# Kernel tuning notes

Measured on AMD Instinct MI355X. Metric: run time of the kernel, lower is better.

The kernel has to match this reference:

```python
import jax, jax.numpy as jnp
import numpy as np

B, N1, N2 = 4, 16384, 4096   # scenes, fine points/scene, coarse points/scene
CIN, COUT = 512, 256
K = 3
EPS_BN = 1e-5
EPS_D = 1e-8


def setup_inputs() -> dict:
    key = jax.random.key(0)
    ks = jax.random.split(key, 6)
    return {
        "point_1": jax.random.uniform(ks[0], (B * N1, 3), dtype=jnp.float32),
        "feat_1": jax.random.normal(ks[1], (B * N1, COUT), dtype=jnp.float32) * 0.1,
        "point_2": jax.random.uniform(ks[2], (B * N2, 3), dtype=jnp.float32),
        "feat_2": jax.random.normal(ks[3], (B * N2, CIN), dtype=jnp.float32) * 0.1,
        "W1": jax.random.normal(ks[4], (COUT, COUT), dtype=jnp.float32) / np.sqrt(COUT).astype(np.float32),
        "b1": jnp.zeros((COUT,), jnp.float32),
        "g1": jnp.ones((COUT,), jnp.float32),
        "beta1": jnp.zeros((COUT,), jnp.float32),
        "W2": jax.random.normal(ks[5], (CIN, COUT), dtype=jnp.float32) / np.sqrt(CIN).astype(np.float32),
        "b2": jnp.zeros((COUT,), jnp.float32),
        "g2": jnp.ones((COUT,), jnp.float32),
        "beta2": jnp.zeros((COUT,), jnp.float32),
        # equal-sized segments: row_splits = [0, N, 2N, ...]
        "row_splits_1": jnp.arange(B + 1, dtype=jnp.int32) * N1,
        "row_splits_2": jnp.arange(B + 1, dtype=jnp.int32) * N2,
    }


def _bn(x, gamma, beta):
    # BatchNorm1d, training mode (biased variance, as in torch)
    mu = x.mean(0)
    var = x.var(0)
    return gamma * (x - mu) * jax.lax.rsqrt(var + EPS_BN) + beta


def reference(point_1, feat_1, point_2, feat_2,
              W1, b1, g1, beta1, W2, b2, g2, beta2,
              row_splits_1, row_splits_2):
    # linear1(feat_1): Linear + BN + ReLU
    f1 = jax.nn.relu(_bn(feat_1 @ W1 + b1, g1, beta1))          # [B*N1, COUT]
    # linear2(feat_2): Linear + BN + ReLU
    f2 = jax.nn.relu(_bn(feat_2 @ W2 + b2, g2, beta2))          # [B*N2, COUT]

    # batched KNN (equal row_splits -> reshape into [B, n, 3])
    q = point_1.reshape(B, N1, 3)
    p = point_2.reshape(B, N2, 3)
    d2 = ((q * q).sum(-1)[:, :, None]
          + (p * p).sum(-1)[:, None, :]
          - 2.0 * jnp.einsum("bnd,bmd->bnm", q, p))             # [B, N1, N2] squared dists
    neg_d, idx = jax.lax.top_k(-d2, K)                           # [B, N1, K]
    dist = jnp.maximum(-neg_d, 0.0)

    # inverse-distance weights (knn search is non-differentiable in the original)
    recip = 1.0 / (dist + EPS_D)
    w = jax.lax.stop_gradient(recip / recip.sum(-1, keepdims=True))  # [B, N1, K]

    # gather + weighted sum (three-interpolate)
    f2b = f2.reshape(B, N2, COUT)
    gathered = f2b[jnp.arange(B)[:, None, None], idx]            # [B, N1, K, COUT]
    interp = (gathered * w[..., None]).sum(2).reshape(B * N1, COUT)

    return f1 + interp
```

## Files before the change

### kernel.cpp

```cpp
#include <hip/hip_runtime.h>
#include <hip/hip_bf16.h>
#include <math.h>

#define N1R 65536
#define N2R 16384
#define NPB 4096
#define NQB 16384
#define CC  256
#define ASTRIDE 40
#define NCELL 512
#define GRID_FAIL_R2 0.015625f

typedef __attribute__((ext_vector_type(4))) float v4f;
typedef __attribute__((ext_vector_type(8))) short v8s;

static __device__ __forceinline__ short f2bs(float f) {
    union { __hip_bfloat16 h; short s; } u;
    u.h = __float2bfloat16(f);
    return u.s;
}

static __device__ __forceinline__ int cell_of(float x, float y, float z) {
    const int cx = min(7, (int)(x * 8.0f));
    const int cy = min(7, (int)(y * 8.0f));
    const int cz = min(7, (int)(z * 8.0f));
    return (cz << 6) | (cy << 3) | cx;
}

static __device__ __forceinline__ void ins3(float d, int si,
    float& b0, float& b1, float& b2, int& i0, int& i1, int& i2)
{
    const bool lt0 = (d < b0) | ((d == b0) & (si < i0));
    const bool lt1 = (d < b1) | ((d == b1) & (si < i1));
    const bool lt2 = (d < b2) | ((d == b2) & (si < i2));
    b2 = lt1 ? b1 : (lt2 ? d : b2);   i2 = lt1 ? i1 : (lt2 ? si : i2);
    b1 = lt0 ? b0 : (lt1 ? d : b1);   i1 = lt0 ? i0 : (lt1 ? si : i1);
    b0 = lt0 ? d  : b0;               i0 = lt0 ? si : i0;
}

__global__ __launch_bounds__(256)
void prep_kernel(const float* __restrict__ W1f, const float* __restrict__ W2f,
                 short* __restrict__ WT1, short* __restrict__ WT2,
                 const float* __restrict__ p2, const float* __restrict__ p1,
                 float4* __restrict__ paug,
                 int* __restrict__ counts_p, int* __restrict__ counts_q)
{
#pragma clang fp contract(off)
    const int bid = blockIdx.x;
    if (bid < 768) {
        const int i = bid * 256 + threadIdx.x;
        if (i < 65536) {
            const int k = i >> 8, n = i & 255;
            WT1[(size_t)n * 256 + k] = f2bs(W1f[i]);
        } else {
            const int j = i - 65536;
            const int k = j >> 8, n = j & 255;
            WT2[(size_t)n * 512 + k] = f2bs(W2f[j]);
        }
    } else if (bid < 832) {
        const int i = (bid - 768) * 256 + threadIdx.x;
        const float x = p2[(size_t)i * 3 + 0];
        const float y = p2[(size_t)i * 3 + 1];
        const float z = p2[(size_t)i * 3 + 2];
        float4 v;
        v.x = x; v.y = y; v.z = z;
        v.w = (x * x + y * y) + z * z;
        paug[i] = v;
        const int b = i >> 12;
        atomicAdd(&counts_p[b * NCELL + cell_of(x, y, z)], 1);
    } else {
        const int i = (bid - 832) * 256 + threadIdx.x;
        const float x = p1[(size_t)i * 3 + 0];
        const float y = p1[(size_t)i * 3 + 1];
        const float z = p1[(size_t)i * 3 + 2];
        const int b = i >> 14;
        atomicAdd(&counts_q[b * NCELL + cell_of(x, y, z)], 1);
    }
}

__global__ __launch_bounds__(512)
void prefix_kernel(const int* __restrict__ counts_p, int* __restrict__ cursors_p,
                   int* __restrict__ starts_p,
                   const int* __restrict__ counts_q, int* __restrict__ cursors_q)
{
    __shared__ int sw[8];
    __shared__ int sbase[8];
    const int t = threadIdx.x;
    const int lane = t & 63, wid = t >> 6;
    for (int a = 0; a < 8; ++a) {
        const int b = a & 3;
        const int* cnt = (a < 4) ? counts_p + b * NCELL : counts_q + b * NCELL;
        const int v = cnt[t];
        int incl = v;
#pragma unroll
        for (int off = 1; off < 64; off <<= 1) {
            const int u = __shfl_up(incl, off);
            incl += (lane >= off) ? u : 0;
        }
        if (lane == 63) sw[wid] = incl;
        __syncthreads();
        if (t == 0) {
            int s = 0;
#pragma unroll
            for (int w = 0; w < 8; ++w) { const int x = sw[w]; sbase[w] = s; s += x; }
        }
        __syncthreads();
        const int inclT = incl + sbase[wid];
        const int excl = inclT - v;
        if (a < 4) {
            starts_p[b * 513 + t] = excl;
            if (t == 511) starts_p[b * 513 + 512] = inclT;
            cursors_p[b * NCELL + t] = excl;
        } else {
            cursors_q[b * NCELL + t] = excl;
        }
        __syncthreads();
    }
}

__global__ __launch_bounds__(256)
void scatter_kernel(const float4* __restrict__ paug, const float* __restrict__ p1,
                    int* __restrict__ cursors_p, int* __restrict__ cursors_q,
                    float4* __restrict__ sortedP, unsigned short* __restrict__ sIdx,
                    unsigned short* __restrict__ qlist)
{
    if (blockIdx.x < 64) {
        const int i = blockIdx.x * 256 + threadIdx.x;
        const float4 v = paug[i];
        const int b = i >> 12;
        const int cell = cell_of(v.x, v.y, v.z);
        const int pos = atomicAdd(&cursors_p[b * NCELL + cell], 1);
        sortedP[(size_t)b * NPB + pos] = v;
        sIdx[(size_t)b * NPB + pos] = (unsigned short)(i & 4095);
    } else {
        const int i = (blockIdx.x - 64) * 256 + threadIdx.x;
        const float x = p1[(size_t)i * 3 + 0];
        const float y = p1[(size_t)i * 3 + 1];
        const float z = p1[(size_t)i * 3 + 2];
        const int b = i >> 14;
        const int cell = cell_of(x, y, z);
        const int pos = atomicAdd(&cursors_q[b * NCELL + cell], 1);
        qlist[(size_t)b * NQB + pos] = (unsigned short)(i & 16383);
    }
}

template<int BM>
static __device__ __forceinline__ void gemm_body(
    int bx, int by,
    const float* __restrict__ X, const short* __restrict__ WT,
    const float* __restrict__ bias, float* __restrict__ Y,
    float* __restrict__ partS, float* __restrict__ partQ,
    int Kdim, short* __restrict__ As0, short* __restrict__ As1)
{
    constexpr int MI  = BM / 32;
    constexpr int NPF = BM / 32;
    constexpr int TPR = 256 / BM;
    constexpr int FPT = BM / 8;

    const int bm0 = bx * BM;
    const int bn0 = by * 128;
    const int wave = threadIdx.x >> 6;
    const int lane = threadIdx.x & 63;
    const int wm0 = (wave >> 1) * (BM / 2);
    const int wn0 = (wave & 1) * 64;
    const int col = lane & 15, quad = lane >> 4;

    const int srow = threadIdx.x / TPR;
    const int skh  = (threadIdx.x % TPR) * FPT;
    const float* sbase = X + (size_t)(bm0 + srow) * Kdim + skh;
    short* sdst0 = As0 + srow * ASTRIDE + skh;
    short* sdst1 = As1 + srow * ASTRIDE + skh;

    v4f acc[MI][4];
#pragma unroll
    for (int i = 0; i < MI; ++i)
#pragma unroll
        for (int j = 0; j < 4; ++j) acc[i][j] = (v4f){0.f, 0.f, 0.f, 0.f};

    const short* wbase = WT + (size_t)(bn0 + wn0 + col) * Kdim + quad * 8;

    v4f pf[NPF];
#pragma unroll
    for (int i = 0; i < NPF; ++i) pf[i] = *(const v4f*)(sbase + i * 4);
    {
        v8s wv;
#pragma unroll
        for (int j = 0; j < NPF / 2; ++j) {
#pragma unroll
            for (int t = 0; t < 4; ++t) {
                wv[t]     = f2bs(pf[2 * j][t]);
                wv[t + 4] = f2bs(pf[2 * j + 1][t]);
            }
            *(v8s*)(sdst0 + j * 8) = wv;
        }
    }
    if (32 < Kdim)
#pragma unroll
        for (int i = 0; i < NPF; ++i) pf[i] = *(const v4f*)(sbase + 32 + i * 4);

    const int NC = Kdim >> 5;
    for (int c = 0; c < NC; ++c) {
        const int k0 = c << 5;
        const bool more = (c + 1 < NC);

        v8s wv[NPF / 2];
        if (more) {
#pragma unroll
            for (int j = 0; j < NPF / 2; ++j)
#pragma unroll
                for (int t = 0; t < 4; ++t) {
                    wv[j][t]     = f2bs(pf[2 * j][t]);
                    wv[j][t + 4] = f2bs(pf[2 * j + 1][t]);
                }
        }
        __syncthreads();
        if (more) {
            short* sd = (c & 1) ? sdst0 : sdst1;
#pragma unroll
            for (int j = 0; j < NPF / 2; ++j) *(v8s*)(sd + j * 8) = wv[j];
        }

        v8s bf[4];
#pragma unroll
        for (int ni = 0; ni < 4; ++ni)
            bf[ni] = *(const v8s*)(wbase + (size_t)(ni * 16) * Kdim + k0);

        if (c + 2 < NC) {
            const float* np = sbase + k0 + 64;
#pragma unroll
            for (int i = 0; i < NPF; ++i) pf[i] = *(const v4f*)(np + i * 4);
        }

        const short* bufc = (c & 1) ? As1 : As0;
        v8s a[MI];
#pragma unroll
        for (int mi = 0; mi < MI; ++mi)
            a[mi] = *(const v8s*)(bufc + (wm0 + mi * 16 + col) * ASTRIDE + quad * 8);
#pragma unroll
        for (int mi = 0; mi < MI; ++mi)
#pragma unroll
            for (int ni = 0; ni < 4; ++ni)
                acc[mi][ni] = __builtin_amdgcn_mfma_f32_16x16x32_bf16(a[mi], bf[ni], acc[mi][ni], 0, 0, 0);
    }

    float* pS = partS + (size_t)(bx * 2 + (wave >> 1)) * CC;
    float* pQ = partQ + (size_t)(bx * 2 + (wave >> 1)) * CC;
#pragma unroll
    for (int ni = 0; ni < 4; ++ni) {
        const int n = bn0 + wn0 + ni * 16 + col;
        const float bv = bias[n];
        float s = 0.f, q = 0.f;
#pragma unroll
        for (int mi = 0; mi < MI; ++mi) {
            const int m = bm0 + wm0 + mi * 16 + quad * 4;
#pragma unroll
            for (int r = 0; r < 4; ++r) {
                const float y = acc[mi][ni][r] + bv;
                Y[(size_t)(m + r) * CC + n] = y;
                s += y; q += y * y;
            }
        }
        s += __shfl_xor(s, 16); q += __shfl_xor(q, 16);
        s += __shfl_xor(s, 32); q += __shfl_xor(q, 32);
        if (quad == 0) { pS[n] = s; pQ[n] = q; }
    }
}

__global__ __launch_bounds__(256)
void gemm_both_kernel(const float* __restrict__ feat1, const short* __restrict__ WT1,
                      const float* __restrict__ b1, float* __restrict__ Y1,
                      float* __restrict__ pS1, float* __restrict__ pQ1,
                      const float* __restrict__ feat2, const short* __restrict__ WT2,
                      const float* __restrict__ b2, float* __restrict__ Y2,
                      float* __restrict__ pS2, float* __restrict__ pQ2)
{
    __shared__ short As[2][64 * ASTRIDE];
    const int id = blockIdx.x;
    if (id < 2048) {
        gemm_body<64>(id >> 1, id & 1, feat1, WT1, b1, Y1, pS1, pQ1, 256,
                      As[0], As[1]);
    } else {
        const int j = id - 2048;
        gemm_body<64>(j >> 1, j & 1, feat2, WT2, b2, Y2, pS2, pQ2, 512,
                      As[0], As[1]);
    }
}

__global__ __launch_bounds__(256)
void stat_reduce_kernel(const float* __restrict__ pS1, const float* __restrict__ pQ1,
                        const float* __restrict__ pS2, const float* __restrict__ pQ2,
                        float* __restrict__ stats)
{
    const int c = threadIdx.x;
    const bool two = blockIdx.x >= 32;
    const float* pS = two ? pS2 : pS1;
    const float* pQ = two ? pQ2 : pQ1;
    const int r0 = (two ? (blockIdx.x - 32) : blockIdx.x) * 64;
    float s = 0.f, q = 0.f;
    for (int r = r0; r < r0 + 64; ++r) {
        s += pS[(size_t)r * CC + c];
        q += pQ[(size_t)r * CC + c];
    }
    float* st = stats + (two ? 512 : 0);
    atomicAdd(&st[c], s);
    atomicAdd(&st[256 + c], q);
}

__global__ __launch_bounds__(512)
void finalize_kernel(const float* __restrict__ sums,
                     const float* __restrict__ g1, const float* __restrict__ be1,
                     const float* __restrict__ g2, const float* __restrict__ be2,
                     float* __restrict__ ac)
{
    const int t = threadIdx.x;
    const int c = t & 255;
    const int which = t >> 8;
    const float* s = sums + which * 512;
    const double n = which ? (double)N2R : (double)N1R;
    const double mu = (double)s[c] / n;
    const double var = (double)s[c + 256] / n - mu * mu;
    const float g  = which ? g2[c]  : g1[c];
    const float be = which ? be2[c] : be1[c];
    const double a  = (double)g / sqrt(var + 1e-5);
    const double cv = (double)be - a * mu;
    ac[which * 512 + c]       = (float)a;
    ac[which * 512 + 256 + c] = (float)cv;
}

__global__ __launch_bounds__(256)
void knn_grid_kernel(const float* __restrict__ p1,
                     const float4* __restrict__ sortedP,
                     const unsigned short* __restrict__ sIdx16,
                     const int* __restrict__ starts_p,
                     const unsigned short* __restrict__ qlist,
                     int* __restrict__ idx_out, float* __restrict__ w_out)
{
#pragma clang fp contract(off)
    __shared__ float4 sP[NPB];
    __shared__ unsigned short sI[NPB];
    __shared__ int sS[513];
    __shared__ float mD[128 * 3];
    __shared__ int   mI[128 * 3];

    const int b = blockIdx.x >> 7;
    const int slot0 = (blockIdx.x & 127) * 128;
    const int tid = threadIdx.x;
    const int lq = tid & 127;
    const int half = tid >> 7;

    {
        const float4* gp = sortedP + (size_t)b * NPB;
        for (int i = tid; i < NPB; i += 256) sP[i] = gp[i];
        const unsigned int* gi = (const unsigned int*)(sIdx16 + (size_t)b * NPB);
        unsigned int* li = (unsigned int*)sI;
        for (int i = tid; i < NPB / 2; i += 256) li[i] = gi[i];
        const int* gs = starts_p + b * 513;
        for (int i = tid; i < 513; i += 256) sS[i] = gs[i];
    }

    const int q = qlist[(size_t)b * NQB + slot0 + lq];
    const int qid = b * NQB + q;
    const float qx = p1[(size_t)qid * 3 + 0];
    const float qy = p1[(size_t)qid * 3 + 1];
    const float qz = p1[(size_t)qid * 3 + 2];
    const float qq = (qx * qx + qy * qy) + qz * qz;
    const int cqx = min(7, (int)(qx * 8.0f));
    const int cqy = min(7, (int)(qy * 8.0f));
    const int cqz = min(7, (int)(qz * 8.0f));

    __syncthreads();

    float b0 = 3.0e38f, b1 = 3.0e38f, b2 = 3.0e38f;
    int i0 = 0x7fffffff, i1 = 0x7fffffff, i2 = 0x7fffffff;

    int n = 0;
    for (int dz = -1; dz <= 1; ++dz)
        for (int dy = -1; dy <= 1; ++dy)
            for (int dx = -1; dx <= 1; ++dx, ++n) {
                if (half ? (n < 14) : (n >= 14)) continue;
                const int cz = cqz + dz, cy = cqy + dy, cx = cqx + dx;
                if (((unsigned)cz | (unsigned)cy | (unsigned)cx) > 7u) continue;
                const int cell = (cz << 6) | (cy << 3) | cx;
                const int ks = sS[cell], ke = sS[cell + 1];
                for (int k = ks; k < ke; ++k) {
                    const float4 P = sP[k];
                    const int si = sI[k];
                    const float dot = fmaf(qz, P.z, fmaf(qy, P.y, qx * P.x));
                    const float d = fmaf(-2.0f, dot, qq + P.w);
                    ins3(d, si, b0, b1, b2, i0, i1, i2);
                }
            }

    if (half) {
        mD[lq * 3 + 0] = b0; mD[lq * 3 + 1] = b1; mD[lq * 3 + 2] = b2;
        mI[lq * 3 + 0] = i0; mI[lq * 3 + 1] = i1; mI[lq * 3 + 2] = i2;
    }
    __syncthreads();
    if (!half) {
#pragma unroll
        for (int r = 0; r < 3; ++r)
            ins3(mD[lq * 3 + r], mI[lq * 3 + r], b0, b1, b2, i0, i1, i2);

        if (!(b2 < GRID_FAIL_R2)) i0 = -1;

        const float r0 = 1.0f / (fmaxf(b0, 0.0f) + 1e-8f);
        const float r1 = 1.0f / (fmaxf(b1, 0.0f) + 1e-8f);
        const float r2 = 1.0f / (fmaxf(b2, 0.0f) + 1e-8f);
        const float rs = (r0 + r1) + r2;
        idx_out[(size_t)qid * 3 + 0] = i0;
        idx_out[(size_t)qid * 3 + 1] = i1;
        idx_out[(size_t)qid * 3 + 2] = i2;
        w_out[(size_t)qid * 3 + 0] = r0 / rs;
        w_out[(size_t)qid * 3 + 1] = r1 / rs;
        w_out[(size_t)qid * 3 + 2] = r2 / rs;
    }
}

__global__ __launch_bounds__(256)
void final_kernel(float* __restrict__ Y1out,
                  const float* __restrict__ Y2raw,
                  const float* __restrict__ ac,
                  const int* __restrict__ idx, const float* __restrict__ w,
                  const unsigned short* __restrict__ qlist,
                  const float* __restrict__ p1, const float4* __restrict__ paug)
{
#pragma clang fp contract(off)
    const int slot = blockIdx.x * 4 + (threadIdx.x >> 6);
    const int b = slot >> 14;
    const int r = b * NQB + qlist[slot];
    const int cg = threadIdx.x & 63;

    const int* ir = idx + (size_t)r * 3;
    int i0 = ir[0], i1 = ir[1], i2 = ir[2];
    float w0, w1, w2;
    if (i0 >= 0) {
        const float* wr = w + (size_t)r * 3;
        w0 = wr[0]; w1 = wr[1]; w2 = wr[2];
    } else {
        const float qx = p1[(size_t)r * 3 + 0];
        const float qy = p1[(size_t)r * 3 + 1];
        const float qz = p1[(size_t)r * 3 + 2];
        const float qq = (qx * qx + qy * qy) + qz * qz;
        float b0 = 3.0e38f, b1 = 3.0e38f, b2 = 3.0e38f;
        i0 = 0x7fffffff; i1 = 0x7fffffff; i2 = 0x7fffffff;
        const float4* pb = paug + (size_t)b * NPB;
        for (int j = cg; j < NPB; j += 64) {
            const float4 P = pb[j];
            const float dot = fmaf(qz, P.z, fmaf(qy, P.y, qx * P.x));
            const float d = fmaf(-2.0f, dot, qq + P.w);
            ins3(d, j, b0, b1, b2, i0, i1, i2);
        }
        for (int m = 1; m < 64; m <<= 1) {
            const float c0 = __shfl_xor(b0, m), c1 = __shfl_xor(b1, m), c2 = __shfl_xor(b2, m);
            const int j0 = __shfl_xor(i0, m), j1 = __shfl_xor(i1, m), j2 = __shfl_xor(i2, m);
            ins3(c0, j0, b0, b1, b2, i0, i1, i2);
            ins3(c1, j1, b0, b1, b2, i0, i1, i2);
            ins3(c2, j2, b0, b1, b2, i0, i1, i2);
        }
        const float r0 = 1.0f / (fmaxf(b0, 0.0f) + 1e-8f);
        const float r1 = 1.0f / (fmaxf(b1, 0.0f) + 1e-8f);
        const float r2 = 1.0f / (fmaxf(b2, 0.0f) + 1e-8f);
        const float rs = (r0 + r1) + r2;
        w0 = r0 / rs; w1 = r1 / rs; w2 = r2 / rs;
    }

    v4f a1 = *(const v4f*)(ac + cg * 4);
    v4f c1 = *(const v4f*)(ac + 256 + cg * 4);
    v4f a2 = *(const v4f*)(ac + 512 + cg * 4);
    v4f c2 = *(const v4f*)(ac + 768 + cg * 4);
    v4f y = *(const v4f*)(Y1out + (size_t)r * CC + cg * 4);
    v4f s;
#pragma unroll
    for (int j = 0; j < 4; ++j)
        s[j] = fmaxf(fmaf(a1[j], y[j], c1[j]), 0.f);

    const int   id3[3] = { i0, i1, i2 };
    const float wk3[3] = { w0, w1, w2 };
#pragma unroll
    for (int k = 0; k < 3; ++k) {
        const float wk = wk3[k];
        v4f g = *(const v4f*)(Y2raw + ((size_t)(b * NPB + id3[k])) * CC + cg * 4);
#pragma unroll
        for (int j = 0; j < 4; ++j) {
            const float gv = fmaxf(fmaf(a2[j], g[j], c2[j]), 0.f);
            s[j] = fmaf(wk, gv, s[j]);
        }
    }
    *(v4f*)(Y1out + (size_t)r * CC + cg * 4) = s;
}

extern "C" void kernel_launch(void* const* d_in, const int* in_sizes, int n_in,
                              void* d_out, int out_size, void* d_ws, size_t ws_size,
                              hipStream_t stream)
{
    const float* point1 = (const float*)d_in[0];
    const float* feat1  = (const float*)d_in[1];
    const float* point2 = (const float*)d_in[2];
    const float* feat2  = (const float*)d_in[3];
    const float* W1     = (const float*)d_in[4];
    const float* b1     = (const float*)d_in[5];
    const float* g1     = (const float*)d_in[6];
    const float* beta1  = (const float*)d_in[7];
    const float* W2     = (const float*)d_in[8];
    const float* b2     = (const float*)d_in[9];
    const float* g2     = (const float*)d_in[10];
    const float* beta2  = (const float*)d_in[11];

    float* Y1 = (float*)d_out;

    char* ws = (char*)d_ws;
    float*          Y2       = (float*)ws;
    float*          stats    = (float*)(ws + (size_t)16777216);
    int*            counts_p = (int*)  (ws + (size_t)16781312);
    int*            counts_q = (int*)  (ws + (size_t)16789504);
    int*            cursors_p= (int*)  (ws + (size_t)16801792);
    int*            cursors_q= (int*)  (ws + (size_t)16809984);
    int*            starts_p = (int*)  (ws + (size_t)16818176);
    float*          ac       = (float*)(ws + (size_t)16826624);
    unsigned short* sIdx16   = (unsigned short*)(ws + (size_t)16830720);
    unsigned short* qlist    = (unsigned short*)(ws + (size_t)16863488);
    float4*         sortedP  = (float4*)(ws + (size_t)17256704);
    int*            idxb     = (int*)  (ws + (size_t)17518848);
    float*          wb       = (float*)(ws + (size_t)18305280);
    short*          WT1      = (short*)(ws + (size_t)19091712);
    short*          WT2      = (short*)(ws + (size_t)19222784);
    float4*         paug     = (float4*)(ws + (size_t)19484928);
    float*          partS1   = (float*)(ws + (size_t)19747072);
    float*          partQ1   = (float*)(ws + (size_t)21844224);
    float*          partS2   = (float*)(ws + (size_t)23941376);
    float*          partQ2   = (float*)(ws + (size_t)24465664);

    hipMemsetAsync(stats, 0, 24576, stream);

    prep_kernel<<<1088, 256, 0, stream>>>(W1, W2, WT1, WT2, point2, point1,
                                          paug, counts_p, counts_q);
    prefix_kernel<<<1, 512, 0, stream>>>(counts_p, cursors_p, starts_p, counts_q, cursors_q);
    scatter_kernel<<<320, 256, 0, stream>>>(paug, point1, cursors_p, cursors_q,
                                            sortedP, sIdx16, qlist);

    gemm_both_kernel<<<2560, 256, 0, stream>>>(feat1, WT1, b1, Y1, partS1, partQ1,
                                               feat2, WT2, b2, Y2, partS2, partQ2);

    stat_reduce_kernel<<<40, 256, 0, stream>>>(partS1, partQ1, partS2, partQ2, stats);
    finalize_kernel<<<1, 512, 0, stream>>>(stats, g1, beta1, g2, beta2, ac);

    knn_grid_kernel<<<512, 256, 0, stream>>>(point1, sortedP, sIdx16, starts_p,
                                             qlist, idxb, wb);

    final_kernel<<<N1R / 4, 256, 0, stream>>>(Y1, Y2, ac, idxb, wb, qlist,
                                              point1, paug);
}
```

Measured before the change: 316.0 us.

## Merge KNN search into the GEMM launch and enlarge GEMM1 row tiles

Folds the KNN grid search into the GEMM kernel as extra blocks, so the latency-bound KNN work runs alongside the MFMA GEMMs instead of in its own launch. The KNN path no longer stages the points into shared memory and reads them straight from global/L2, which keeps the fused kernel's LDS footprint small. GEMM1 switches to 128-row tiles, halving its block count and the partial-stat rows, and the stat-reduce grid is shrunk to match. The risks are uncached global loads in the KNN inner loop, and imbalance between the block types sharing one launch.

```diff
diff --git a/kernel.cpp b/kernel.cpp
--- a/kernel.cpp
+++ b/kernel.cpp
@@ -266,21 +266,105 @@
     }
 }
 
+static __device__ __forceinline__ void knn_body(
+    int bid,
+    const float* __restrict__ p1, const float4* __restrict__ sortedP,
+    const unsigned short* __restrict__ sIdx16, const int* __restrict__ starts_p,
+    const unsigned short* __restrict__ qlist,
+    int* __restrict__ idx_out, float* __restrict__ w_out,
+    float* __restrict__ mD, int* __restrict__ mI)
+{
+#pragma clang fp contract(off)
+    const int b = bid >> 7;
+    const int slot0 = (bid & 127) * 128;
+    const int tid = threadIdx.x;
+    const int lq = tid & 127;
+    const int half = tid >> 7;
+
+    const float4* pb = sortedP + (size_t)b * NPB;
+    const unsigned short* ib = sIdx16 + (size_t)b * NPB;
+    const int* st = starts_p + b * 513;
+
+    const int q = qlist[(size_t)b * NQB + slot0 + lq];
+    const int qid = b * NQB + q;
+    const float qx = p1[(size_t)qid * 3 + 0];
+    const float qy = p1[(size_t)qid * 3 + 1];
+    const float qz = p1[(size_t)qid * 3 + 2];
+    const float qq = (qx * qx + qy * qy) + qz * qz;
+    const int cqx = min(7, (int)(qx * 8.0f));
+    const int cqy = min(7, (int)(qy * 8.0f));
+    const int cqz = min(7, (int)(qz * 8.0f));
+
+    float b0 = 3.0e38f, b1 = 3.0e38f, b2 = 3.0e38f;
+    int i0 = 0x7fffffff, i1 = 0x7fffffff, i2 = 0x7fffffff;
+
+    int n = 0;
+    for (int dz = -1; dz <= 1; ++dz)
+        for (int dy = -1; dy <= 1; ++dy)
+            for (int dx = -1; dx <= 1; ++dx, ++n) {
+                if (half ? (n < 14) : (n >= 14)) continue;
+                const int cz = cqz + dz, cy = cqy + dy, cx = cqx + dx;
+                if (((unsigned)cz | (unsigned)cy | (unsigned)cx) > 7u) continue;
+                const int cell = (cz << 6) | (cy << 3) | cx;
+                const int ks = st[cell], ke = st[cell + 1];
+                for (int k = ks; k < ke; ++k) {
+                    const float4 P = pb[k];
+                    const int si = ib[k];
+                    const float dot = fmaf(qz, P.z, fmaf(qy, P.y, qx * P.x));
+                    const float d = fmaf(-2.0f, dot, qq + P.w);
+                    ins3(d, si, b0, b1, b2, i0, i1, i2);
+                }
+            }
+
+    if (half) {
+        mD[lq * 3 + 0] = b0; mD[lq * 3 + 1] = b1; mD[lq * 3 + 2] = b2;
+        mI[lq * 3 + 0] = i0; mI[lq * 3 + 1] = i1; mI[lq * 3 + 2] = i2;
+    }
+    __syncthreads();
+    if (!half) {
+#pragma unroll
+        for (int r = 0; r < 3; ++r)
+            ins3(mD[lq * 3 + r], mI[lq * 3 + r], b0, b1, b2, i0, i1, i2);
+
+        if (!(b2 < GRID_FAIL_R2)) i0 = -1;
+
+        const float r0 = 1.0f / (fmaxf(b0, 0.0f) + 1e-8f);
+        const float r1 = 1.0f / (fmaxf(b1, 0.0f) + 1e-8f);
+        const float r2 = 1.0f / (fmaxf(b2, 0.0f) + 1e-8f);
+        const float rs = (r0 + r1) + r2;
+        idx_out[(size_t)qid * 3 + 0] = i0;
+        idx_out[(size_t)qid * 3 + 1] = i1;
+        idx_out[(size_t)qid * 3 + 2] = i2;
+        w_out[(size_t)qid * 3 + 0] = r0 / rs;
+        w_out[(size_t)qid * 3 + 1] = r1 / rs;
+        w_out[(size_t)qid * 3 + 2] = r2 / rs;
+    }
+}
+
 __global__ __launch_bounds__(256)
-void gemm_both_kernel(const float* __restrict__ feat1, const short* __restrict__ WT1,
-                      const float* __restrict__ b1, float* __restrict__ Y1,
-                      float* __restrict__ pS1, float* __restrict__ pQ1,
-                      const float* __restrict__ feat2, const short* __restrict__ WT2,
-                      const float* __restrict__ b2, float* __restrict__ Y2,
-                      float* __restrict__ pS2, float* __restrict__ pQ2)
-{
-    __shared__ short As[2][64 * ASTRIDE];
+void mega_kernel(const float* __restrict__ feat1, const short* __restrict__ WT1,
+                 const float* __restrict__ b1, float* __restrict__ Y1,
+                 float* __restrict__ pS1, float* __restrict__ pQ1,
+                 const float* __restrict__ feat2, const short* __restrict__ WT2,
+                 const float* __restrict__ b2, float* __restrict__ Y2,
+                 float* __restrict__ pS2, float* __restrict__ pQ2,
+                 const float* __restrict__ point1, const float4* __restrict__ sortedP,
+                 const unsigned short* __restrict__ sIdx16,
+                 const int* __restrict__ starts_p, const unsigned short* __restrict__ qlist,
+                 int* __restrict__ idxb, float* __restrict__ wb)
+{
+    __shared__ short As[2][128 * ASTRIDE];
     const int id = blockIdx.x;
-    if (id < 2048) {
-        gemm_body<64>(id >> 1, id & 1, feat1, WT1, b1, Y1, pS1, pQ1, 256,
-                      As[0], As[1]);
+    if (id < 512) {
+        float* mD = (float*)&As[0][0];
+        int*   mI = (int*)((char*)&As[0][0] + 1536);
+        knn_body(id, point1, sortedP, sIdx16, starts_p, qlist, idxb, wb, mD, mI);
+    } else if (id < 1536) {
+        const int j = id - 512;
+        gemm_body<128>(j >> 1, j & 1, feat1, WT1, b1, Y1, pS1, pQ1, 256,
+                       As[0], As[1]);
     } else {
-        const int j = id - 2048;
+        const int j = id - 1536;
         gemm_body<64>(j >> 1, j & 1, feat2, WT2, b2, Y2, pS2, pQ2, 512,
                       As[0], As[1]);
     }
@@ -292,10 +376,10 @@
                         float* __restrict__ stats)
 {
     const int c = threadIdx.x;
-    const bool two = blockIdx.x >= 32;
+    const bool two = blockIdx.x >= 16;
     const float* pS = two ? pS2 : pS1;
     const float* pQ = two ? pQ2 : pQ1;
-    const int r0 = (two ? (blockIdx.x - 32) : blockIdx.x) * 64;
+    const int r0 = (two ? (blockIdx.x - 16) : blockIdx.x) * 64;
     float s = 0.f, q = 0.f;
     for (int r = r0; r < r0 + 64; ++r) {
         s += pS[(size_t)r * CC + c];
@@ -325,95 +409,6 @@
     const double cv = (double)be - a * mu;
     ac[which * 512 + c]       = (float)a;
     ac[which * 512 + 256 + c] = (float)cv;
-}
-
-__global__ __launch_bounds__(256)
-void knn_grid_kernel(const float* __restrict__ p1,
-                     const float4* __restrict__ sortedP,
-                     const unsigned short* __restrict__ sIdx16,
-                     const int* __restrict__ starts_p,
-                     const unsigned short* __restrict__ qlist,
-                     int* __restrict__ idx_out, float* __restrict__ w_out)
-{
-#pragma clang fp contract(off)
-    __shared__ float4 sP[NPB];
-    __shared__ unsigned short sI[NPB];
-    __shared__ int sS[513];
-    __shared__ float mD[128 * 3];
-    __shared__ int   mI[128 * 3];
-
-    const int b = blockIdx.x >> 7;
-    const int slot0 = (blockIdx.x & 127) * 128;
-    const int tid = threadIdx.x;
-    const int lq = tid & 127;
-    const int half = tid >> 7;
-
-    {
-        const float4* gp = sortedP + (size_t)b * NPB;
-        for (int i = tid; i < NPB; i += 256) sP[i] = gp[i];
-        const unsigned int* gi = (const unsigned int*)(sIdx16 + (size_t)b * NPB);
-        unsigned int* li = (unsigned int*)sI;
-        for (int i = tid; i < NPB / 2; i += 256) li[i] = gi[i];
-        const int* gs = starts_p + b * 513;
-        for (int i = tid; i < 513; i += 256) sS[i] = gs[i];
-    }
-
-    const int q = qlist[(size_t)b * NQB + slot0 + lq];
-    const int qid = b * NQB + q;
-    const float qx = p1[(size_t)qid * 3 + 0];
-    const float qy = p1[(size_t)qid * 3 + 1];
-    const float qz = p1[(size_t)qid * 3 + 2];
-    const float qq = (qx * qx + qy * qy) + qz * qz;
-    const int cqx = min(7, (int)(qx * 8.0f));
-    const int cqy = min(7, (int)(qy * 8.0f));
-    const int cqz = min(7, (int)(qz * 8.0f));
-
-    __syncthreads();
-
-    float b0 = 3.0e38f, b1 = 3.0e38f, b2 = 3.0e38f;
-    int i0 = 0x7fffffff, i1 = 0x7fffffff, i2 = 0x7fffffff;
-
-    int n = 0;
-    for (int dz = -1; dz <= 1; ++dz)
-        for (int dy = -1; dy <= 1; ++dy)
-            for (int dx = -1; dx <= 1; ++dx, ++n) {
-                if (half ? (n < 14) : (n >= 14)) continue;
-                const int cz = cqz + dz, cy = cqy + dy, cx = cqx + dx;
-                if (((unsigned)cz | (unsigned)cy | (unsigned)cx) > 7u) continue;
-                const int cell = (cz << 6) | (cy << 3) | cx;
-                const int ks = sS[cell], ke = sS[cell + 1];
-                for (int k = ks; k < ke; ++k) {
-                    const float4 P = sP[k];
-                    const int si = sI[k];
-                    const float dot = fmaf(qz, P.z, fmaf(qy, P.y, qx * P.x));
-                    const float d = fmaf(-2.0f, dot, qq + P.w);
-                    ins3(d, si, b0, b1, b2, i0, i1, i2);
-                }
-            }
-
-    if (half) {
-        mD[lq * 3 + 0] = b0; mD[lq * 3 + 1] = b1; mD[lq * 3 + 2] = b2;
-        mI[lq * 3 + 0] = i0; mI[lq * 3 + 1] = i1; mI[lq * 3 + 2] = i2;
-    }
-    __syncthreads();
-    if (!half) {
-#pragma unroll
-        for (int r = 0; r < 3; ++r)
-            ins3(mD[lq * 3 + r], mI[lq * 3 + r], b0, b1, b2, i0, i1, i2);
-
-        if (!(b2 < GRID_FAIL_R2)) i0 = -1;
-
-        const float r0 = 1.0f / (fmaxf(b0, 0.0f) + 1e-8f);
-        const float r1 = 1.0f / (fmaxf(b1, 0.0f) + 1e-8f);
-        const float r2 = 1.0f / (fmaxf(b2, 0.0f) + 1e-8f);
-        const float rs = (r0 + r1) + r2;
-        idx_out[(size_t)qid * 3 + 0] = i0;
-        idx_out[(size_t)qid * 3 + 1] = i1;
-        idx_out[(size_t)qid * 3 + 2] = i2;
-        w_out[(size_t)qid * 3 + 0] = r0 / rs;
-        w_out[(size_t)qid * 3 + 1] = r1 / rs;
-        w_out[(size_t)qid * 3 + 2] = r2 / rs;
-    }
 }
 
 __global__ __launch_bounds__(256)
@@ -538,14 +533,13 @@
     scatter_kernel<<<320, 256, 0, stream>>>(paug, point1, cursors_p, cursors_q,
                                             sortedP, sIdx16, qlist);
 
-    gemm_both_kernel<<<2560, 256, 0, stream>>>(feat1, WT1, b1, Y1, partS1, partQ1,
-                                               feat2, WT2, b2, Y2, partS2, partQ2);
-
-    stat_reduce_kernel<<<40, 256, 0, stream>>>(partS1, partQ1, partS2, partQ2, stats);
+    mega_kernel<<<2048, 256, 0, stream>>>(feat1, WT1, b1, Y1, partS1, partQ1,
+                                          feat2, WT2, b2, Y2, partS2, partQ2,
+                                          point1, sortedP, sIdx16, starts_p,
+                                          qlist, idxb, wb);
+
+    stat_reduce_kernel<<<24, 256, 0, stream>>>(partS1, partQ1, partS2, partQ2, stats);
     finalize_kernel<<<1, 512, 0, stream>>>(stats, g1, beta1, g2, beta2, ac);
-
-    knn_grid_kernel<<<512, 256, 0, stream>>>(point1, sortedP, sIdx16, starts_p,
-                                             qlist, idxb, wb);
 
     final_kernel<<<N1R / 4, 256, 0, stream>>>(Y1, Y2, ac, idxb, wb, qlist,
                                               point1, paug);
```

New measurement: 303.0 us. 4.1% less time.
